# Optimization experiments

Hardware: AMD Instinct MI355X
Metric: run time of the kernel (lower is better)

The kernel has to match this reference:

```python
import math
import jax, jax.numpy as jnp
import numpy as np

HEADS = 8
D = 128            # model_dim
PE = D // 2        # position_embedding_size (query_positional_score=True)
MAXP = 32          # max_position_embeddings
LN_EPS = 1e-5


def setup_inputs() -> dict:
    key = jax.random.key(0)
    ks = jax.random.split(key, 7)
    bs, h, w = 8, 32, 32
    hidden_state = jax.random.normal(ks[0], (bs, h, w, D), dtype=jnp.float32)
    row_emb = jax.random.normal(ks[1], (2 * MAXP - 1, PE), dtype=jnp.float32) * 0.02
    col_emb = jax.random.normal(ks[2], (2 * MAXP - 1, PE), dtype=jnp.float32) * 0.02
    # torch Linear weights are (out_features, in_features)
    Wq = jax.random.normal(ks[3], (HEADS * D, D), dtype=jnp.float32) / math.sqrt(D)
    Wk = jax.random.normal(ks[4], (HEADS * D, D), dtype=jnp.float32) / math.sqrt(D)
    Wv = jax.random.normal(ks[5], (D, HEADS * D), dtype=jnp.float32) / math.sqrt(HEADS * D)
    bv = jnp.zeros((D,), dtype=jnp.float32)
    ln_g = jnp.ones((D,), dtype=jnp.float32)
    ln_b = jnp.zeros((D,), dtype=jnp.float32)
    return {"hidden_state": hidden_state, "row_emb": row_emb, "col_emb": col_emb,
            "Wq": Wq, "Wk": Wk, "Wv": Wv, "bv": bv, "ln_g": ln_g, "ln_b": ln_b}


def _layer_norm(x, g, b):
    mu = jnp.mean(x, axis=-1, keepdims=True)
    var = jnp.var(x, axis=-1, keepdims=True)
    return (x - mu) * jax.lax.rsqrt(var + LN_EPS) * g + b


def _forward(hidden_state, row_emb, col_emb, Wq, Wk, Wv, bv, ln_g, ln_b):
    bs, h, w, _ = hidden_state.shape
    x = _layer_norm(hidden_state, ln_g, ln_b)  # pre_norm=True
    sqrt_norm = math.sqrt(D)

    # relative indices (static, h == w == 32 here)
    deltas = np.arange(MAXP)[None, :] - np.arange(MAXP)[:, None]
    rel = deltas + MAXP - 1
    row_embeds = row_emb[rel[:w, :w]]  # (w, w, PE)
    col_embeds = col_emb[rel[:h, :h]]  # (h, h, PE)

    # projections; original does .view(bs, w, h, heads, D) on a (bs,h,w,heads*D) tensor
    q = jnp.einsum('bhwc,oc->bhwo', x, Wq).reshape(bs, w, h, HEADS, D)
    k = jnp.einsum('bhwc,oc->bhwo', x, Wk).reshape(bs, w, h, HEADS, D)

    q_row = q[..., :PE]
    q_col = q[..., PE:]
    row_scores = jnp.einsum('bijhd,ikd->bijhk', q_row, row_embeds)
    col_scores = jnp.einsum('bijhd,jld->bijhl', q_col, col_embeds)
    scores = (row_scores[..., :, None] + col_scores[..., None, :]) / sqrt_norm  # bijhkl
    scores = scores.transpose(0, 2, 1, 3, 5, 4)

    content = jnp.einsum('bijhd,bklhd->bijhkl', q, k) / sqrt_norm
    scores = scores + content.transpose(0, 2, 1, 3, 5, 4)  # (bs, h, w, heads, h, w)

    attn_shape = scores.shape
    probs = jax.nn.softmax(scores.reshape(*attn_shape[:-2], -1), axis=-1).reshape(attn_shape)

    # dropout omitted (inference / p=0)
    context = jnp.einsum('bijhkl,bkld->bijhd', probs, x)
    context = context.reshape(bs, h, w, HEADS * D)
    output = jnp.einsum('bhwc,oc->bhwo', context, Wv) + bv + x
    return output, probs


def reference(hidden_state, row_emb, col_emb, Wq, Wk, Wv, bv, ln_g, ln_b):
    return _forward(hidden_state, row_emb, col_emb, Wq, Wk, Wv, bv, ln_g, ln_b)
```

## Files before the change

### kernel.cpp

```cpp
#include <hip/hip_runtime.h>
#include <hip/hip_bf16.h>

#define HEADS 8
#define D 128
#define QSCALE 0.12751743f

typedef unsigned short u16;
typedef unsigned int u32;
typedef __attribute__((ext_vector_type(8))) short short8;
typedef __attribute__((ext_vector_type(4))) float f32x4;

static __device__ inline u16 f2bf(float f) {
    u32 u = __float_as_uint(f);
    return (u16)((u + 0x7FFFu + ((u >> 16) & 1u)) >> 16);
}
static __device__ inline u32 pk2bf(float a, float b) {
    return (u32)f2bf(a) | ((u32)f2bf(b) << 16);
}
static __device__ inline f32x4 mfma16(short8 a, short8 b, f32x4 c) {
    return __builtin_amdgcn_mfma_f32_16x16x32_bf16(a, b, c, 0, 0, 0);
}
static __device__ inline short8 cvt8(const float* e) {
    f32x4 v0 = *(const f32x4*)e;
    f32x4 v1 = *(const f32x4*)(e + 4);
    union { uint4 u; short8 s; } x;
    x.u = make_uint4(pk2bf(v0[0], v0[1]), pk2bf(v0[2], v0[3]),
                     pk2bf(v1[0], v1[1]), pk2bf(v1[2], v1[3]));
    return x.s;
}

__global__ __launch_bounds__(256) void k_wcvt(const float* __restrict__ Wq,
    const float* __restrict__ Wk, const float* __restrict__ Wv,
    u16* __restrict__ wqk, u16* __restrict__ wv)
{
    int idx = (blockIdx.x * 256 + threadIdx.x) * 4;
    const float* src;
    u16* dst;
    if (idx < 131072)      { src = Wq + idx;           dst = wqk + idx; }
    else if (idx < 262144) { src = Wk + (idx - 131072); dst = wqk + idx; }
    else                   { src = Wv + (idx - 262144); dst = wv + (idx - 262144); }
    f32x4 v = *(const f32x4*)src;
    *(uint2*)dst = make_uint2(pk2bf(v[0], v[1]), pk2bf(v[2], v[3]));
}

__global__ __launch_bounds__(256) void k_ln(const float* __restrict__ hs,
    const float* __restrict__ g, const float* __restrict__ b,
    float* __restrict__ xf, u16* __restrict__ xbf)
{
    int row  = blockIdx.x * 4 + (threadIdx.x >> 6);
    int lane = threadIdx.x & 63;
    const float* p = hs + (size_t)row * D + lane * 2;
    float2 v = *(const float2*)p;
    float s  = v.x + v.y;
    float s2 = v.x * v.x + v.y * v.y;
    #pragma unroll
    for (int off = 1; off < 64; off <<= 1) {
        s  += __shfl_xor(s, off);
        s2 += __shfl_xor(s2, off);
    }
    float mu  = s * 0.0078125f;
    float var = s2 * 0.0078125f - mu * mu;
    float inv = rsqrtf(var + 1e-5f);
    float2 o;
    o.x = (v.x - mu) * inv * g[lane * 2 + 0] + b[lane * 2 + 0];
    o.y = (v.y - mu) * inv * g[lane * 2 + 1] + b[lane * 2 + 1];
    *(float2*)(xf + (size_t)row * D + lane * 2) = o;
    *(u32*)(xbf + (size_t)row * D + lane * 2) = pk2bf(o.x, o.y);
}

__global__ __launch_bounds__(256) void k_xt(const float* __restrict__ xf,
    u16* __restrict__ xt)
{
    __shared__ __align__(16) u16 tl[128][136];
    int b = blockIdx.x, ch = blockIdx.y;
    int tid = threadIdx.x;
    const float* src = xf + ((size_t)b * 1024 + ch * 128) * 128;
    #pragma unroll
    for (int it = 0; it < 16; ++it) {
        int s = tid + it * 256;
        int p = s >> 5, d4 = (s & 31) * 4;
        f32x4 v = *(const f32x4*)(src + (size_t)p * 128 + d4);
        tl[d4 + 0][p] = f2bf(v[0]);
        tl[d4 + 1][p] = f2bf(v[1]);
        tl[d4 + 2][p] = f2bf(v[2]);
        tl[d4 + 3][p] = f2bf(v[3]);
    }
    __syncthreads();
    u16* dst = xt + (size_t)b * 131072 + ch * 128;
    #pragma unroll
    for (int i = 0; i < 8; ++i) {
        int d = (tid >> 4) + i * 16, c8 = (tid & 15) * 8;
        *(uint4*)(dst + (size_t)d * 1024 + c8) = *(const uint4*)&tl[d][c8];
    }
}

__global__ __launch_bounds__(256) void k_proj(const u16* __restrict__ xbf,
    const u16* __restrict__ wqk,
    u16* __restrict__ q_bf, u16* __restrict__ kt_bf)
{
    int tid = threadIdx.x;
    int w = tid >> 6, l = tid & 63, h = l >> 4, ln = l & 15;
    int t0 = blockIdx.x * 64 + w * 16;
    int o0 = blockIdx.y * 64;
    short8 a[4];
    #pragma unroll
    for (int s = 0; s < 4; ++s)
        a[s] = *(const short8*)(xbf + (size_t)(t0 + ln) * 128 + s * 32 + h * 8);
    f32x4 acc[4];
    #pragma unroll
    for (int n = 0; n < 4; ++n) acc[n] = f32x4{0.f, 0.f, 0.f, 0.f};
    #pragma unroll
    for (int n = 0; n < 4; ++n) {
        const u16* wsrc = wqk + (size_t)(o0 + n * 16 + ln) * 128;
        #pragma unroll
        for (int s = 0; s < 4; ++s) {
            short8 bf = *(const short8*)(wsrc + s * 32 + h * 8);
            acc[n] = mfma16(a[s], bf, acc[n]);
        }
    }
    bool isq = (o0 < 1024);
    float oscale = isq ? QSCALE : 1.0f;
    int head = (o0 & 1023) >> 7;
    int od_base = (o0 & 127);
    u16* basep = isq ? q_bf : kt_bf;
    #pragma unroll
    for (int n = 0; n < 4; ++n) {
        int d0 = od_base + n * 16 + ln;
        #pragma unroll
        for (int r = 0; r < 4; ++r) {
            int t = t0 + h * 4 + r;
            int b = t >> 10, pos = t & 1023;
            size_t row;
            if (isq) row = (size_t)(b * 8 + head) * 1024 + pos;
            else { int I = pos >> 5, J = pos & 31; row = (size_t)(b * 8 + head) * 1024 + (J * 32 + I); }
            basep[row * 128 + d0] = f2bf(acc[n][r] * oscale);
        }
    }
}

__global__ __launch_bounds__(256) void k_bias(const u16* __restrict__ q_bf,
    const float* __restrict__ row_emb, const float* __restrict__ col_emb,
    float* __restrict__ rbias, float* __restrict__ cbias)
{
    __shared__ __align__(16) float cbf[32][68];
    int tid = threadIdx.x;
    int w = tid >> 6, l = tid & 63, h = l >> 4, ln = l & 15;
    int blk = blockIdx.x;
    int bh = blk >> 5, I = blk & 31;
    const u16* qb = q_bf + ((size_t)bh * 1024 + I * 32) * 128;
    size_t obase = (size_t)blk * 1024;
    if (w < 2) {
        short8 a0 = *(const short8*)(qb + (size_t)(w * 16 + ln) * 128 + h * 8);
        short8 a1 = *(const short8*)(qb + (size_t)(w * 16 + ln) * 128 + 32 + h * 8);
        f32x4 o[2] = {f32x4{0,0,0,0}, f32x4{0,0,0,0}};
        #pragma unroll
        for (int n = 0; n < 2; ++n) {
            int K = n * 16 + ln;
            const float* e = row_emb + (size_t)(K - I + 31) * 64 + h * 8;
            o[n] = mfma16(a0, cvt8(e), o[n]);
            o[n] = mfma16(a1, cvt8(e + 32), o[n]);
        }
        #pragma unroll
        for (int n = 0; n < 2; ++n)
            #pragma unroll
            for (int r = 0; r < 4; ++r)
                rbias[obase + (size_t)(w * 16 + h * 4 + r) * 32 + n * 16 + ln] = o[n][r];
    } else {
        int m = w - 2;
        short8 a0 = *(const short8*)(qb + (size_t)(m * 16 + ln) * 128 + 64 + h * 8);
        short8 a1 = *(const short8*)(qb + (size_t)(m * 16 + ln) * 128 + 96 + h * 8);
        f32x4 o[4] = {f32x4{0,0,0,0}, f32x4{0,0,0,0}, f32x4{0,0,0,0}, f32x4{0,0,0,0}};
        #pragma unroll
        for (int n = 0; n < 4; ++n) {
            int p = n * 16 + ln;
            if (p > 62) p = 62;
            const float* e = col_emb + (size_t)p * 64 + h * 8;
            o[n] = mfma16(a0, cvt8(e), o[n]);
            o[n] = mfma16(a1, cvt8(e + 32), o[n]);
        }
        #pragma unroll
        for (int n = 0; n < 4; ++n)
            #pragma unroll
            for (int r = 0; r < 4; ++r)
                cbf[m * 16 + h * 4 + r][n * 16 + ln] = o[n][r];
    }
    __syncthreads();
    int J = tid >> 3, L0 = (tid & 7) * 4;
    float4 g;
    g.x = cbf[J][L0 + 0 - J + 31];
    g.y = cbf[J][L0 + 1 - J + 31];
    g.z = cbf[J][L0 + 2 - J + 31];
    g.w = cbf[J][L0 + 3 - J + 31];
    *(float4*)(cbias + obase + (size_t)J * 32 + L0) = g;
}

__global__ __launch_bounds__(512, 4) void k_attn(const u16* __restrict__ q_bf,
    const u16* __restrict__ kt_bf, const u16* __restrict__ xt_bf,
    const float* __restrict__ rbias, const float* __restrict__ cbias,
    float* __restrict__ probs, u16* __restrict__ ctx_bf)
{
    __shared__ __align__(16) char P[65536];
    __shared__ float wred[2][256];
    __shared__ float linv_s[32];

    int tid = threadIdx.x;
    int w = tid >> 6, l = tid & 63, h = l >> 4, ln = l & 15;
    int flat = blockIdx.x;
    int swz = (flat & 7) * 256 + (flat >> 3);
    int bh = swz >> 5, I = swz & 31;
    int b = bh >> 3, head = bh & 7;
    int kk0 = w * 128;

    f32x4 acc[2][8];
    #pragma unroll
    for (int n = 0; n < 2; ++n)
        #pragma unroll
        for (int t = 0; t < 8; ++t) acc[n][t] = f32x4{0.f, 0.f, 0.f, 0.f};
    const u16* kbase = kt_bf + ((size_t)bh * 1024 + kk0) * 128;
    const u16* qbase = q_bf + ((size_t)bh * 1024 + I * 32) * 128;
    #pragma unroll
    for (int s = 0; s < 4; ++s) {
        short8 q0 = *(const short8*)(qbase + (size_t)ln * 128 + s * 32 + h * 8);
        short8 q1 = *(const short8*)(qbase + (size_t)(16 + ln) * 128 + s * 32 + h * 8);
        #pragma unroll
        for (int t = 0; t < 8; ++t) {
            short8 kf = *(const short8*)(kbase + (size_t)(t * 16 + ln) * 128 + s * 32 + h * 8);
            acc[0][t] = mfma16(kf, q0, acc[0][t]);
            acc[1][t] = mfma16(kf, q1, acc[1][t]);
        }
    }

    const float* rbase = rbias + (size_t)(bh * 32 + I) * 1024;
    const float* cbase = cbias + (size_t)(bh * 32 + I) * 1024;
    f32x4 rbr[2][2], cbr[2];
    #pragma unroll
    for (int n = 0; n < 2; ++n) {
        int J = n * 16 + ln;
        rbr[n][0] = *(const f32x4*)(rbase + J * 32 + h * 4);
        rbr[n][1] = *(const f32x4*)(rbase + J * 32 + 16 + h * 4);
        cbr[n]    = *(const f32x4*)(cbase + J * 32 + w * 4);
    }

    #pragma unroll
    for (int n = 0; n < 2; ++n) {
        float mx = -1e30f;
        #pragma unroll
        for (int t = 0; t < 8; ++t) {
            float cbv = cbr[n][t >> 1];
            #pragma unroll
            for (int r = 0; r < 4; ++r) {
                float v = acc[n][t][r] + rbr[n][t & 1][r] + cbv;
                acc[n][t][r] = v;
                mx = fmaxf(mx, v);
            }
        }
        mx = fmaxf(mx, __shfl_xor(mx, 16));
        mx = fmaxf(mx, __shfl_xor(mx, 32));
        if (l < 16) wred[0][w * 32 + n * 16 + ln] = mx;
    }
    __syncthreads();

    #pragma unroll
    for (int n = 0; n < 2; ++n) {
        int J = n * 16 + ln;
        float M = wred[0][J];
        #pragma unroll
        for (int w2 = 1; w2 < 8; ++w2) M = fmaxf(M, wred[0][w2 * 32 + J]);
        float sum = 0.f;
        #pragma unroll
        for (int t = 0; t < 8; ++t) {
            float p0 = exp2f(acc[n][t][0] - M);
            float p1 = exp2f(acc[n][t][1] - M);
            float p2 = exp2f(acc[n][t][2] - M);
            float p3 = exp2f(acc[n][t][3] - M);
            acc[n][t] = f32x4{p0, p1, p2, p3};
            sum += (p0 + p1) + (p2 + p3);
            int kk = kk0 + t * 16 + h * 4;
            *(uint2*)(P + J * 2048 + ((kk * 2) ^ ((J & 7) << 4))) =
                make_uint2(pk2bf(p0, p1), pk2bf(p2, p3));
        }
        sum += __shfl_xor(sum, 16);
        sum += __shfl_xor(sum, 32);
        if (l < 16) wred[1][w * 32 + J] = sum;
    }
    __syncthreads();
    if (tid < 32) {
        float s = 0.f;
        #pragma unroll
        for (int w2 = 0; w2 < 8; ++w2) s += wred[1][w2 * 32 + tid];
        linv_s[tid] = 1.0f / s;
    }
    __syncthreads();

    #pragma unroll
    for (int n = 0; n < 2; ++n) {
        int J = n * 16 + ln;
        float inv = linv_s[J];
        float* prow = probs + ((((size_t)(b * 32 + J) * 32 + I) * 8 + head) << 10)
                    + kk0 + h * 4;
        #pragma unroll
        for (int t = 0; t < 8; ++t) {
            *(float4*)(prow + t * 16) = make_float4(
                acc[n][t][0] * inv, acc[n][t][1] * inv,
                acc[n][t][2] * inv, acc[n][t][3] * inv);
        }
    }

    f32x4 cacc[2] = {f32x4{0,0,0,0}, f32x4{0,0,0,0}};
    int d0 = w * 16;
    const u16* xb = xt_bf + (size_t)b * 131072 + (size_t)(d0 + ln) * 1024 + h * 8;
    #pragma unroll 4
    for (int ks = 0; ks < 32; ++ks) {
        short8 xf8 = *(const short8*)(xb + ks * 32);
        #pragma unroll
        for (int m = 0; m < 2; ++m) {
            int J = m * 16 + ln;
            short8 pa = *(const short8*)(P + J * 2048 +
                (((ks * 32 + h * 8) * 2) ^ ((J & 7) << 4)));
            cacc[m] = mfma16(pa, xf8, cacc[m]);
        }
    }
    #pragma unroll
    for (int m = 0; m < 2; ++m)
        #pragma unroll
        for (int r = 0; r < 4; ++r) {
            int J = m * 16 + h * 4 + r;
            ctx_bf[((size_t)(b * 32 + J) * 32 + I) * 1024 + head * 128 + d0 + ln] =
                f2bf(cacc[m][r] * linv_s[J]);
        }
}

__global__ __launch_bounds__(256) void k_out(const u16* __restrict__ ctx_bf,
    const u16* __restrict__ wv_bf, const float* __restrict__ bv,
    const float* __restrict__ xf, float* __restrict__ out)
{
    int tid = threadIdx.x;
    int w = tid >> 6, l = tid & 63, h = l >> 4, ln = l & 15;
    int wm = w >> 1, wn = w & 1;
    int t0 = blockIdx.x * 32 + wm * 16;
    int o0 = blockIdx.y * 64 + wn * 32;
    f32x4 acc[2] = {f32x4{0,0,0,0}, f32x4{0,0,0,0}};
    for (int ks = 0; ks < 32; ++ks) {
        short8 a = *(const short8*)(ctx_bf + (size_t)(t0 + ln) * 1024 + ks * 32 + h * 8);
        #pragma unroll
        for (int nt = 0; nt < 2; ++nt) {
            short8 bb = *(const short8*)(wv_bf + (size_t)(o0 + nt * 16 + ln) * 1024 + ks * 32 + h * 8);
            acc[nt] = mfma16(a, bb, acc[nt]);
        }
    }
    #pragma unroll
    for (int nt = 0; nt < 2; ++nt) {
        int o = o0 + nt * 16 + ln;
        float bvv = bv[o];
        #pragma unroll
        for (int r = 0; r < 4; ++r) {
            int t = t0 + h * 4 + r;
            out[(size_t)t * 128 + o] = acc[nt][r] + bvv + xf[(size_t)t * 128 + o];
        }
    }
}

extern "C" void kernel_launch(void* const* d_in, const int* in_sizes, int n_in,
                              void* d_out, int out_size, void* d_ws, size_t ws_size,
                              hipStream_t stream) {
    (void)in_sizes; (void)n_in; (void)out_size; (void)ws_size;
    const float* hs      = (const float*)d_in[0];
    const float* row_emb = (const float*)d_in[1];
    const float* col_emb = (const float*)d_in[2];
    const float* Wq      = (const float*)d_in[3];
    const float* Wk      = (const float*)d_in[4];
    const float* Wv      = (const float*)d_in[5];
    const float* bv      = (const float*)d_in[6];
    const float* ln_g    = (const float*)d_in[7];
    const float* ln_b    = (const float*)d_in[8];

    float* out   = (float*)d_out;
    float* probs = out + 1048576;

    char* ws = (char*)d_ws;
    float* xf     = (float*)(ws);
    u16*   xbf    = (u16*)(ws + 4194304);
    u16*   q_bf   = (u16*)(ws + 6291456);
    u16*   kt_bf  = (u16*)(ws + 23068672);
    u16*   xt     = (u16*)(ws + 39845888);
    u16*   wqk_bf = (u16*)(ws + 41943040);
    u16*   wv_bf  = (u16*)(ws + 42467328);
    u16*   ctx    = (u16*)(ws + 42729472);
    float* rbias  = (float*)(ws + 59506688);
    float* cbias  = (float*)(ws + 67895296);

    k_wcvt <<<384, 256, 0, stream>>>(Wq, Wk, Wv, wqk_bf, wv_bf);
    k_ln   <<<2048, 256, 0, stream>>>(hs, ln_g, ln_b, xf, xbf);
    k_xt   <<<dim3(8, 8), 256, 0, stream>>>(xf, xt);
    k_proj <<<dim3(128, 32), 256, 0, stream>>>(xbf, wqk_bf, q_bf, kt_bf);
    k_bias <<<2048, 256, 0, stream>>>(q_bf, row_emb, col_emb, rbias, cbias);
    k_attn <<<2048, 512, 0, stream>>>(q_bf, kt_bf, xt, rbias, cbias, probs, ctx);
    k_out  <<<dim3(256, 2), 256, 0, stream>>>(ctx, wv_bf, bv, xf, out);
}
```

Before: 276.5 us.

## Halve attention LDS tile by processing query rows in two passes

The attention kernel's shared P buffer shrinks from 64KB to 32KB. The two 16-row halves of probabilities are staged and multiplied against x one after the other, with an extra pair of barriers between them, and the launch bound asks for 8 blocks per CU instead of 4. The block-index swizzle is removed, the bias loads are moved ahead of the QK MFMAs, and bf16 packing now uses the hardware-conversion intrinsic. The aim is higher occupancy and better latency hiding. The cost is serialising the PV phase, re-reading the x tiles twice, and possible register spills under the tighter bound.

After: 636.0 us. 130% more time.

```diff
diff --git a/kernel.cpp b/kernel.cpp
--- a/kernel.cpp
+++ b/kernel.cpp
@@ -16,6 +16,11 @@
 }
 static __device__ inline u32 pk2bf(float a, float b) {
     return (u32)f2bf(a) | ((u32)f2bf(b) << 16);
+}
+static __device__ inline u32 cvtpk(float a, float b) {
+    union { __hip_bfloat162 h; u32 u; } x;
+    x.h = __float22bfloat162_rn(make_float2(a, b));
+    return x.u;
 }
 static __device__ inline f32x4 mfma16(short8 a, short8 b, f32x4 c) {
     return __builtin_amdgcn_mfma_f32_16x16x32_bf16(a, b, c, 0, 0, 0);
@@ -194,41 +199,21 @@
     *(float4*)(cbias + obase + (size_t)J * 32 + L0) = g;
 }
 
-__global__ __launch_bounds__(512, 4) void k_attn(const u16* __restrict__ q_bf,
+__global__ __launch_bounds__(512, 8) void k_attn(const u16* __restrict__ q_bf,
     const u16* __restrict__ kt_bf, const u16* __restrict__ xt_bf,
     const float* __restrict__ rbias, const float* __restrict__ cbias,
     float* __restrict__ probs, u16* __restrict__ ctx_bf)
 {
-    __shared__ __align__(16) char P[65536];
+    __shared__ __align__(16) char P[32768];
     __shared__ float wred[2][256];
     __shared__ float linv_s[32];
 
     int tid = threadIdx.x;
     int w = tid >> 6, l = tid & 63, h = l >> 4, ln = l & 15;
     int flat = blockIdx.x;
-    int swz = (flat & 7) * 256 + (flat >> 3);
-    int bh = swz >> 5, I = swz & 31;
+    int bh = flat >> 5, I = flat & 31;
     int b = bh >> 3, head = bh & 7;
     int kk0 = w * 128;
-
-    f32x4 acc[2][8];
-    #pragma unroll
-    for (int n = 0; n < 2; ++n)
-        #pragma unroll
-        for (int t = 0; t < 8; ++t) acc[n][t] = f32x4{0.f, 0.f, 0.f, 0.f};
-    const u16* kbase = kt_bf + ((size_t)bh * 1024 + kk0) * 128;
-    const u16* qbase = q_bf + ((size_t)bh * 1024 + I * 32) * 128;
-    #pragma unroll
-    for (int s = 0; s < 4; ++s) {
-        short8 q0 = *(const short8*)(qbase + (size_t)ln * 128 + s * 32 + h * 8);
-        short8 q1 = *(const short8*)(qbase + (size_t)(16 + ln) * 128 + s * 32 + h * 8);
-        #pragma unroll
-        for (int t = 0; t < 8; ++t) {
-            short8 kf = *(const short8*)(kbase + (size_t)(t * 16 + ln) * 128 + s * 32 + h * 8);
-            acc[0][t] = mfma16(kf, q0, acc[0][t]);
-            acc[1][t] = mfma16(kf, q1, acc[1][t]);
-        }
-    }
 
     const float* rbase = rbias + (size_t)(bh * 32 + I) * 1024;
     const float* cbase = cbias + (size_t)(bh * 32 + I) * 1024;
@@ -239,6 +224,25 @@
         rbr[n][0] = *(const f32x4*)(rbase + J * 32 + h * 4);
         rbr[n][1] = *(const f32x4*)(rbase + J * 32 + 16 + h * 4);
         cbr[n]    = *(const f32x4*)(cbase + J * 32 + w * 4);
+    }
+
+    f32x4 acc[2][8];
+    #pragma unroll
+    for (int n = 0; n < 2; ++n)
+        #pragma unroll
+        for (int t = 0; t < 8; ++t) acc[n][t] = f32x4{0.f, 0.f, 0.f, 0.f};
+    const u16* kbase = kt_bf + ((size_t)bh * 1024 + kk0) * 128;
+    const u16* qbase = q_bf + ((size_t)bh * 1024 + I * 32) * 128;
+    #pragma unroll
+    for (int s = 0; s < 4; ++s) {
+        short8 q0 = *(const short8*)(qbase + (size_t)ln * 128 + s * 32 + h * 8);
+        short8 q1 = *(const short8*)(qbase + (size_t)(16 + ln) * 128 + s * 32 + h * 8);
+        #pragma unroll
+        for (int t = 0; t < 8; ++t) {
+            short8 kf = *(const short8*)(kbase + (size_t)(t * 16 + ln) * 128 + s * 32 + h * 8);
+            acc[0][t] = mfma16(kf, q0, acc[0][t]);
+            acc[1][t] = mfma16(kf, q1, acc[1][t]);
+        }
     }
 
     #pragma unroll
@@ -275,9 +279,11 @@
             float p3 = exp2f(acc[n][t][3] - M);
             acc[n][t] = f32x4{p0, p1, p2, p3};
             sum += (p0 + p1) + (p2 + p3);
-            int kk = kk0 + t * 16 + h * 4;
-            *(uint2*)(P + J * 2048 + ((kk * 2) ^ ((J & 7) << 4))) =
-                make_uint2(pk2bf(p0, p1), pk2bf(p2, p3));
+            if (n == 0) {
+                int kk = kk0 + t * 16 + h * 4;
+                *(uint2*)(P + ln * 2048 + ((kk * 2) ^ ((ln & 7) << 4))) =
+                    make_uint2(cvtpk(p0, p1), cvtpk(p2, p3));
+            }
         }
         sum += __shfl_xor(sum, 16);
         sum += __shfl_xor(sum, 32);
@@ -292,42 +298,68 @@
     }
     __syncthreads();
 
-    #pragma unroll
-    for (int n = 0; n < 2; ++n) {
-        int J = n * 16 + ln;
-        float inv = linv_s[J];
-        float* prow = probs + ((((size_t)(b * 32 + J) * 32 + I) * 8 + head) << 10)
-                    + kk0 + h * 4;
-        #pragma unroll
-        for (int t = 0; t < 8; ++t) {
-            *(float4*)(prow + t * 16) = make_float4(
-                acc[n][t][0] * inv, acc[n][t][1] * inv,
-                acc[n][t][2] * inv, acc[n][t][3] * inv);
-        }
-    }
-
-    f32x4 cacc[2] = {f32x4{0,0,0,0}, f32x4{0,0,0,0}};
     int d0 = w * 16;
     const u16* xb = xt_bf + (size_t)b * 131072 + (size_t)(d0 + ln) * 1024 + h * 8;
-    #pragma unroll 4
-    for (int ks = 0; ks < 32; ++ks) {
-        short8 xf8 = *(const short8*)(xb + ks * 32);
-        #pragma unroll
-        for (int m = 0; m < 2; ++m) {
-            int J = m * 16 + ln;
-            short8 pa = *(const short8*)(P + J * 2048 +
-                (((ks * 32 + h * 8) * 2) ^ ((J & 7) << 4)));
-            cacc[m] = mfma16(pa, xf8, cacc[m]);
-        }
-    }
-    #pragma unroll
-    for (int m = 0; m < 2; ++m)
+
+    {
+        float inv = linv_s[ln];
+        float* prow = probs + ((((size_t)(b * 32 + ln) * 32 + I) * 8 + head) << 10)
+                    + kk0 + h * 4;
+        #pragma unroll
+        for (int t = 0; t < 8; ++t) {
+            f32x4 o = acc[0][t];
+            *(f32x4*)(prow + t * 16) = f32x4{o[0] * inv, o[1] * inv, o[2] * inv, o[3] * inv};
+        }
+        f32x4 cacc = f32x4{0.f, 0.f, 0.f, 0.f};
+        #pragma unroll 4
+        for (int ks = 0; ks < 32; ++ks) {
+            short8 xf8 = *(const short8*)(xb + ks * 32);
+            short8 pa = *(const short8*)(P + ln * 2048 +
+                (((ks * 32 + h * 8) * 2) ^ ((ln & 7) << 4)));
+            cacc = mfma16(pa, xf8, cacc);
+        }
         #pragma unroll
         for (int r = 0; r < 4; ++r) {
-            int J = m * 16 + h * 4 + r;
+            int J = h * 4 + r;
             ctx_bf[((size_t)(b * 32 + J) * 32 + I) * 1024 + head * 128 + d0 + ln] =
-                f2bf(cacc[m][r] * linv_s[J]);
-        }
+                f2bf(cacc[r] * linv_s[J]);
+        }
+    }
+    __syncthreads();
+
+    #pragma unroll
+    for (int t = 0; t < 8; ++t) {
+        int kk = kk0 + t * 16 + h * 4;
+        *(uint2*)(P + ln * 2048 + ((kk * 2) ^ ((ln & 7) << 4))) =
+            make_uint2(cvtpk(acc[1][t][0], acc[1][t][1]),
+                       cvtpk(acc[1][t][2], acc[1][t][3]));
+    }
+    __syncthreads();
+
+    {
+        float inv = linv_s[16 + ln];
+        float* prow = probs + ((((size_t)(b * 32 + 16 + ln) * 32 + I) * 8 + head) << 10)
+                    + kk0 + h * 4;
+        #pragma unroll
+        for (int t = 0; t < 8; ++t) {
+            f32x4 o = acc[1][t];
+            *(f32x4*)(prow + t * 16) = f32x4{o[0] * inv, o[1] * inv, o[2] * inv, o[3] * inv};
+        }
+        f32x4 cacc = f32x4{0.f, 0.f, 0.f, 0.f};
+        #pragma unroll 4
+        for (int ks = 0; ks < 32; ++ks) {
+            short8 xf8 = *(const short8*)(xb + ks * 32);
+            short8 pa = *(const short8*)(P + ln * 2048 +
+                (((ks * 32 + h * 8) * 2) ^ ((ln & 7) << 4)));
+            cacc = mfma16(pa, xf8, cacc);
+        }
+        #pragma unroll
+        for (int r = 0; r < 4; ++r) {
+            int J = 16 + h * 4 + r;
+            ctx_bf[((size_t)(b * 32 + J) * 32 + I) * 1024 + head * 128 + d0 + ln] =
+                f2bf(cacc[r] * linv_s[J]);
+        }
+    }
 }
 
 __global__ __launch_bounds__(256) void k_out(const u16* __restrict__ ctx_bf,
```
